# Kernel optimization log

Measured on AMD Instinct MI355X. Metric: run time of the kernel, lower is better.

The kernel has to match this reference:

```python
import jax, jax.numpy as jnp
import numpy as np

ALPHA = 0.2  # LeakyReLU negative slope


def setup_inputs() -> dict:
    key = jax.random.key(0)
    k1, k2, k3, k4 = jax.random.split(key, 4)
    B, T, D_in, H, S = 32, 1024, 64, 64, 2
    embedding = jax.random.normal(k1, (B, T, D_in), dtype=jnp.float32)
    x = jax.random.normal(k2, (S * B, T, D_in), dtype=jnp.float32)
    # xavier_uniform-ish scale for params
    W = jax.random.normal(k3, (D_in, H), dtype=jnp.float32) * (1.414 * np.sqrt(2.0 / (D_in + H)))
    a = jax.random.normal(k4, (2 * H, 1), dtype=jnp.float32) * (1.414 * np.sqrt(2.0 / (2 * H + 1)))
    return {"embedding": embedding, "x": x, "W": W, "a": a, "input_size": S}


def reference(embedding, x, W, a, input_size):
    # embedding: [B, T, D_in], W: [D_in, H], a: [2H, 1], x: [S*B, T, D_in]
    H = W.shape[1]
    h = jnp.einsum("btd,dh->bth", embedding, W)          # [B, T, H]
    a1 = a[:H, 0]                                        # attends to h_i (query side)
    a2 = a[H:, 0]                                        # attends to h_j (key side)
    f1 = h @ a1                                          # [B, T]
    f2 = h @ a2                                          # [B, T]
    # e_ij = leakyrelu(a1.h_i + a2.h_j) -- avoids materializing [B,T,T,2H]
    e = jax.nn.leaky_relu(f1[:, :, None] + f2[:, None, :], negative_slope=ALPHA)  # [B, T, T]
    attn = jax.nn.softmax(e, axis=2)                     # [B, T, T]
    attn_tiled = jnp.tile(attn, (input_size, 1, 1))      # [S*B, T, T] (dropout: eval mode, identity)
    out = jnp.einsum("bij,bjd->bid", attn_tiled, x)      # [S*B, T, D_in]
    return out
```

## Files before the change

kernel.cpp:

```cpp
#include <hip/hip_runtime.h>

typedef float  f32x4 __attribute__((ext_vector_type(4)));
typedef _Float16 h16x8 __attribute__((ext_vector_type(8)));
typedef _Float16 h16x2 __attribute__((ext_vector_type(2)));

#define LOG2E 1.4426950408889634f
#define ALPHA 0.2f

__device__ __forceinline__ float fexp2(float v) {
#if __has_builtin(__builtin_amdgcn_exp2f)
  return __builtin_amdgcn_exp2f(v);
#else
  return exp2f(v);
#endif
}

__global__ __launch_bounds__(256) void fkern(
    const float* __restrict__ emb, const float* __restrict__ W,
    const float* __restrict__ a, float* __restrict__ f1, float* __restrict__ f2)
{
  __shared__ float w1s[64], w2s[64];
  const int t = threadIdx.x;
  if (t < 128) {
    const int d = t & 63;
    const float* wrow = W + d * 64;
    const float* av = a + (t >> 6) * 64;
    float s = 0.f;
#pragma unroll
    for (int h = 0; h < 64; ++h) s = fmaf(wrow[h], av[h], s);
    if (t < 64) w1s[d] = s; else w2s[d] = s;
  }
  __syncthreads();
  const int R = blockIdx.x * 64 + (t >> 2);
  const int q = t & 3;
  const f32x4* er = (const f32x4*)(emb + (size_t)R * 64 + q * 16);
  float s1 = 0.f, s2 = 0.f;
#pragma unroll
  for (int r = 0; r < 4; ++r) {
    f32x4 v = er[r];
#pragma unroll
    for (int c = 0; c < 4; ++c) {
      s1 = fmaf(v[c], w1s[q * 16 + r * 4 + c], s1);
      s2 = fmaf(v[c], w2s[q * 16 + r * 4 + c], s2);
    }
  }
  s1 += __shfl_xor(s1, 1); s1 += __shfl_xor(s1, 2);
  s2 += __shfl_xor(s2, 1); s2 += __shfl_xor(s2, 2);
  if (q == 0) { f1[R] = s1 * LOG2E; f2[R] = s2 * LOG2E; }
}

__global__ __launch_bounds__(1024, 1) void attn_main(
    const float* __restrict__ x, const float* __restrict__ f1g,
    const float* __restrict__ f2g, float* __restrict__ out)
{
  __shared__ __attribute__((aligned(16))) _Float16 Xt[2][128 * 128];
  __shared__ float e1s[1024], e2s[1024];
  __shared__ float red[16];

  const int t    = threadIdx.x;
  const int wid  = t >> 6;
  const int lane = t & 63;
  const int l15  = lane & 15;
  const int g    = lane >> 4;
  const int wc   = wid & 1;
  const int wr   = wid >> 1;
  const int b    = blockIdx.x >> 3;
  const int brow = (blockIdx.x & 7) * 128;

  float rv[16];

  auto stage_loads = [&](int kc) {
#pragma unroll
    for (int p = 0; p < 2; ++p) {
      const int pp = wid * 2 + p;
      const int h  = pp >> 4;
      const int j0 = (pp & 15) * 8;
      const float* base = x + (size_t)(b + 32 * h) * 65536
                            + (size_t)(kc * 128 + j0 + 2 * g) * 64 + l15;
#pragma unroll
      for (int i = 0; i < 4; ++i) {
        rv[p * 8 + i]     = base[i * 16];
        rv[p * 8 + 4 + i] = base[64 + i * 16];
      }
    }
  };
  auto stage_writes = [&](int buf) {
#pragma unroll
    for (int p = 0; p < 2; ++p) {
      const int pp = wid * 2 + p;
      const int h  = pp >> 4;
      const int k8 = pp & 15;
#pragma unroll
      for (int i = 0; i < 4; ++i) {
        const int row = h * 64 + l15 + 16 * i;
        const int kb  = k8 ^ (row & 7);
        h16x2 hp;
        hp[0] = (_Float16)rv[p * 8 + i];
        hp[1] = (_Float16)rv[p * 8 + 4 + i];
        *(unsigned*)&Xt[buf][row * 128 + kb * 8 + 2 * g] = __builtin_bit_cast(unsigned, hp);
      }
    }
  };

  stage_loads(0);

  {
    const float v = f2g[b * 1024 + t];
    e1s[t] = fexp2(v);
    e2s[t] = fexp2(ALPHA * v);
    float m = v;
#pragma unroll
    for (int off = 1; off < 64; off <<= 1) m = fmaxf(m, __shfl_xor(m, off));
    if (lane == 0) red[wid] = m;
  }
  const float f1v = f1g[b * 1024 + brow + wr * 16 + l15];
  __syncthreads();
  float mf2 = red[0];
#pragma unroll
  for (int i = 1; i < 16; ++i) mf2 = fmaxf(mf2, red[i]);
  const float u  = f1v + mf2;
  const float mL = fmaxf(u, ALPHA * u);
  const float CA = fexp2(f1v - mL);
  const float CB = fexp2(fmaf(ALPHA, f1v, -mL));
  stage_writes(0);
  __syncthreads();

  f32x4 acc[4] = {};
  f32x4 accz = {};
  h16x8 ones;
#pragma unroll
  for (int i = 0; i < 8; ++i) ones[i] = (_Float16)1.0f;

  const int l7 = l15 & 7;

  for (int kc = 0; kc < 8; ++kc) {
    const int buf = kc & 1;
    if (kc < 7) stage_loads(kc + 1);
#pragma unroll
    for (int ks = 0; ks < 4; ++ks) {
      const int jb = kc * 128 + ks * 32 + g * 8;
      f32x4 e1a = *(const f32x4*)(e1s + jb);
      f32x4 e1b = *(const f32x4*)(e1s + jb + 4);
      f32x4 e2a = *(const f32x4*)(e2s + jb);
      f32x4 e2b = *(const f32x4*)(e2s + jb + 4);
      float ev1[8], ev2[8];
#pragma unroll
      for (int i = 0; i < 4; ++i) {
        ev1[i] = e1a[i]; ev1[4 + i] = e1b[i];
        ev2[i] = e2a[i]; ev2[4 + i] = e2b[i];
      }
      h16x8 a0;
#pragma unroll
      for (int jj = 0; jj < 4; ++jj) {
        float p0 = fmaxf(CA * ev1[2 * jj],     CB * ev2[2 * jj]);
        float p1 = fmaxf(CA * ev1[2 * jj + 1], CB * ev2[2 * jj + 1]);
        h16x2 pk = __builtin_bit_cast(h16x2, __builtin_amdgcn_cvt_pkrtz(p0, p1));
        a0[2 * jj] = pk[0]; a0[2 * jj + 1] = pk[1];
      }
#pragma unroll
      for (int nf = 0; nf < 4; ++nf) {
        const int row = wc * 64 + nf * 16 + l15;
        const int kb  = (ks * 4 + g) ^ l7;
        h16x8 bf = *(const h16x8*)&Xt[buf][row * 128 + kb * 8];
        acc[nf] = __builtin_amdgcn_mfma_f32_16x16x32_f16(a0, bf, acc[nf], 0, 0, 0);
      }
      accz = __builtin_amdgcn_mfma_f32_16x16x32_f16(a0, ones, accz, 0, 0, 0);
    }
    if (kc < 7) stage_writes(buf ^ 1);
    __syncthreads();
  }

  float rz[4];
#pragma unroll
  for (int r = 0; r < 4; ++r) rz[r] = 1.0f / accz[r];
  const int i0 = brow + wr * 16;
  const int bo = b + 32 * wc;
  float* op = out + (size_t)bo * 65536;
#pragma unroll
  for (int nf = 0; nf < 4; ++nf) {
    const int n = nf * 16 + l15;
#pragma unroll
    for (int r = 0; r < 4; ++r) {
      op[(size_t)(i0 + g * 4 + r) * 64 + n] = acc[nf][r] * rz[r];
    }
  }
}

extern "C" void kernel_launch(void* const* d_in, const int* in_sizes, int n_in,
                              void* d_out, int out_size, void* d_ws, size_t ws_size,
                              hipStream_t stream) {
  const float* emb = (const float*)d_in[0];
  const float* x   = (const float*)d_in[1];
  const float* W   = (const float*)d_in[2];
  const float* a   = (const float*)d_in[3];
  float* f1 = (float*)d_ws;
  float* f2 = f1 + 32 * 1024;
  fkern<<<512, 256, 0, stream>>>(emb, W, a, f1, f2);
  attn_main<<<256, 1024, 0, stream>>>(x, f1, f2, (float*)d_out);
}
```

Baseline: 38.34 us.

## Vectorize x staging loads with shuffle transpose and remap block order

The x tile loads change from scalar per-lane loads to 16-byte vector loads per lane. Lanes then exchange values with cross-lane shuffles so each thread can pack four fp16 values and write them to the swizzled transposed LDS tile in one 8-byte store. Block indexing is remapped so consecutive blocks cover different batches instead of row chunks of the same batch. In the small projection kernel, W is first staged into padded shared memory. The shuffles add ALU work, and the new index mapping is complex enough to risk a layout mismatch.

After: 40.82 us. +6.5%, slower.

```diff
diff --git a/kernel.cpp b/kernel.cpp
--- a/kernel.cpp
+++ b/kernel.cpp
@@ -3,6 +3,7 @@
 typedef float  f32x4 __attribute__((ext_vector_type(4)));
 typedef _Float16 h16x8 __attribute__((ext_vector_type(8)));
 typedef _Float16 h16x2 __attribute__((ext_vector_type(2)));
+typedef unsigned uintx2 __attribute__((ext_vector_type(2)));
 
 #define LOG2E 1.4426950408889634f
 #define ALPHA 0.2f
@@ -19,15 +20,21 @@
     const float* __restrict__ emb, const float* __restrict__ W,
     const float* __restrict__ a, float* __restrict__ f1, float* __restrict__ f2)
 {
+  __shared__ float Ws[64 * 65];
   __shared__ float w1s[64], w2s[64];
   const int t = threadIdx.x;
+#pragma unroll
+  for (int i = 0; i < 16; ++i) {
+    const int idx = i * 256 + t;
+    Ws[(idx >> 6) * 65 + (idx & 63)] = W[idx];
+  }
+  __syncthreads();
   if (t < 128) {
     const int d = t & 63;
-    const float* wrow = W + d * 64;
     const float* av = a + (t >> 6) * 64;
     float s = 0.f;
 #pragma unroll
-    for (int h = 0; h < 64; ++h) s = fmaf(wrow[h], av[h], s);
+    for (int h = 0; h < 64; ++h) s = fmaf(Ws[d * 65 + h], av[h], s);
     if (t < 64) w1s[d] = s; else w2s[d] = s;
   }
   __syncthreads();
@@ -64,41 +71,40 @@
   const int g    = lane >> 4;
   const int wc   = wid & 1;
   const int wr   = wid >> 1;
-  const int b    = blockIdx.x >> 3;
-  const int brow = (blockIdx.x & 7) * 128;
-
-  float rv[16];
+  const int b    = blockIdx.x & 31;
+  const int brow = (blockIdx.x >> 5) * 128;
+
+  const int R2 = g >> 1, u2 = g & 1;
+
+  f32x4 rv[4];
 
   auto stage_loads = [&](int kc) {
 #pragma unroll
-    for (int p = 0; p < 2; ++p) {
-      const int pp = wid * 2 + p;
-      const int h  = pp >> 4;
-      const int j0 = (pp & 15) * 8;
-      const float* base = x + (size_t)(b + 32 * h) * 65536
-                            + (size_t)(kc * 128 + j0 + 2 * g) * 64 + l15;
-#pragma unroll
-      for (int i = 0; i < 4; ++i) {
-        rv[p * 8 + i]     = base[i * 16];
-        rv[p * 8 + 4 + i] = base[64 + i * 16];
-      }
+    for (int c = 0; c < 4; ++c) {
+      const int h = c >> 1;
+      const int j = (c & 1) * 64 + wid * 4 + g;
+      const float* p = x + (size_t)(b + 32 * h) * 65536
+                         + (size_t)(kc * 128 + j) * 64 + l15 * 4;
+      rv[c] = *(const f32x4*)p;
     }
   };
   auto stage_writes = [&](int buf) {
 #pragma unroll
-    for (int p = 0; p < 2; ++p) {
-      const int pp = wid * 2 + p;
-      const int h  = pp >> 4;
-      const int k8 = pp & 15;
-#pragma unroll
-      for (int i = 0; i < 4; ++i) {
-        const int row = h * 64 + l15 + 16 * i;
-        const int kb  = k8 ^ (row & 7);
-        h16x2 hp;
-        hp[0] = (_Float16)rv[p * 8 + i];
-        hp[1] = (_Float16)rv[p * 8 + 4 + i];
-        *(unsigned*)&Xt[buf][row * 128 + kb * 8 + 2 * g] = __builtin_bit_cast(unsigned, hp);
-      }
+    for (int c = 0; c < 4; ++c) {
+      f32x4 v = rv[c];
+      float e0 = __shfl_xor(R2 ? v[0] : v[2], 32);
+      float e1 = __shfl_xor(R2 ? v[1] : v[3], 32);
+      if (R2) { v[0] = e0; v[1] = e1; } else { v[2] = e0; v[3] = e1; }
+      float q0 = __shfl_xor(u2 ? v[0] : v[1], 16);
+      float q1 = __shfl_xor(u2 ? v[2] : v[3], 16);
+      if (u2) { v[0] = q0; v[2] = q1; } else { v[1] = q0; v[3] = q1; }
+      uintx2 w;
+      w[0] = __builtin_bit_cast(unsigned, __builtin_amdgcn_cvt_pkrtz(v[0], v[1]));
+      w[1] = __builtin_bit_cast(unsigned, __builtin_amdgcn_cvt_pkrtz(v[2], v[3]));
+      const int row = (c >> 1) * 64 + l15 * 4 + g;
+      const int k8  = (c & 1) * 8 + (wr >> 0 ? 0 : 0) + (wid >> 1);
+      const int kb  = k8 ^ (row & 7);
+      *(uintx2*)&Xt[buf][row * 128 + kb * 8 + (wid & 1) * 4] = w;
     }
   };
 
```
